# Optimization experiments

Hardware: AMD Instinct MI355X
Metric: run time of the kernel (lower is better)

The kernel has to match this reference:

```python
import jax, jax.numpy as jnp
import numpy as np

B, CIN, F, L = 16, 4, 64, 4096
H = CIN * F   # d_model = 256
N = 32        # SSM state size (S4D)

def setup_inputs() -> dict:
    key = jax.random.key(0)
    ks = jax.random.split(key, 9)
    inp = jax.random.normal(ks[0], (B, CIN, F, L), dtype=jnp.float32)
    # S4D parameterization: dt log-uniform in [1e-3, 1e-1], A = -exp(log_A_real) + i*A_imag (S4D-Lin init)
    log_dt = jnp.log(10.0 ** jax.random.uniform(ks[1], (H,), minval=-3.0, maxval=-1.0)).astype(jnp.float32)
    log_A_real = jnp.log(0.5 * jnp.ones((H, N), dtype=jnp.float32))
    A_imag = jnp.broadcast_to(np.pi * jnp.arange(N, dtype=jnp.float32), (H, N)).copy()
    C_real = jax.random.normal(ks[2], (H, N), dtype=jnp.float32) * (0.5 ** 0.5)
    C_imag = jax.random.normal(ks[3], (H, N), dtype=jnp.float32) * (0.5 ** 0.5)
    D = jax.random.normal(ks[4], (H,), dtype=jnp.float32)
    W_out = jax.random.normal(ks[5], (H, H), dtype=jnp.float32) / jnp.sqrt(H).astype(jnp.float32)
    b_out = jnp.zeros((H,), dtype=jnp.float32)
    return {"inp": inp, "log_dt": log_dt, "log_A_real": log_A_real, "A_imag": A_imag,
            "C_real": C_real, "C_imag": C_imag, "D": D, "W_out": W_out, "b_out": b_out}

def _s4d_kernel(log_dt, log_A_real, A_imag, C_real, C_imag, length):
    dt = jnp.exp(log_dt)                              # (H,)
    A = -jnp.exp(log_A_real) + 1j * A_imag            # (H,N) complex
    dtA = A * dt[:, None]                             # (H,N)
    C = C_real + 1j * C_imag                          # (H,N)
    Ct = C * (jnp.exp(dtA) - 1.0) / A                 # ZOH discretization of B*C
    l = jnp.arange(length, dtype=jnp.float32)
    vand = jnp.exp(dtA[:, :, None] * l)               # (H,N,L) Vandermonde of exp(dt*A)
    return 2.0 * jnp.einsum('hn,hnl->hl', Ct, vand).real  # (H,L) float

def reference(inp, log_dt, log_A_real, A_imag, C_real, C_imag, D, W_out, b_out):
    b, cin, f, l = inp.shape
    # transpose(2,3) then transpose(1,2): (B,C,F,L) -> (B,L,C,F) -> reshape (B,L,H)
    x = jnp.transpose(inp, (0, 3, 1, 2)).reshape(b, l, cin * f)
    u = jnp.transpose(x, (0, 2, 1))                   # (B,H,L)
    K = _s4d_kernel(log_dt, log_A_real, A_imag, C_real, C_imag, l)  # (H,L)
    n = 2 * l
    y = jnp.fft.irfft(jnp.fft.rfft(u, n) * jnp.fft.rfft(K, n), n)[..., :l]  # causal conv
    y = y + D[:, None] * u                            # skip connection
    y = jnp.transpose(y, (0, 2, 1))                   # (B,L,H)
    y = jax.nn.gelu(y)                                # S4Block default activation
    y = y @ W_out.T + b_out                           # output linear, final_act='id'
    # transpose(1,2) then reshape: (B,L,H) -> (B,H,L) -> (B,C,F,L)
    return jnp.transpose(y, (0, 2, 1)).reshape(b, cin, f, l)
```

## Files before the change

### kernel.cpp

```cpp
#include <hip/hip_runtime.h>
#include <hip/hip_bf16.h>
#include <cstdint>

#define S4_H 256
#define S4_N 32
#define S4_L 4096
#define S4_B 16
#define S4_T 64
#define S4_C 64

typedef __attribute__((ext_vector_type(8))) short bf16x8;
typedef __attribute__((ext_vector_type(4))) float f32x4;

__device__ __forceinline__ uint32_t s4_f2bf(float f) {
    uint32_t u = __float_as_uint(f);
    return (u + 0x7fffu + ((u >> 16) & 1u)) >> 16;
}

__device__ __forceinline__ float s4_gelu(float x) {
    float x3 = x * x * x;
    float z = 1.5957691216057308f * fmaf(0.044715f, x3, x);
    float e = __expf(-z);
    return x / (1.0f + e);
}

__device__ __forceinline__ float s4_rowsum32(float v) {
    v += __int_as_float(__builtin_amdgcn_update_dpp(0, __float_as_int(v), 0x111, 0xf, 0xf, false));
    v += __int_as_float(__builtin_amdgcn_update_dpp(0, __float_as_int(v), 0x112, 0xf, 0xf, false));
    v += __int_as_float(__builtin_amdgcn_update_dpp(0, __float_as_int(v), 0x114, 0xf, 0xf, false));
    v += __int_as_float(__builtin_amdgcn_update_dpp(0, __float_as_int(v), 0x118, 0xf, 0xf, false));
    v += __int_as_float(__builtin_amdgcn_update_dpp(0, __float_as_int(v), 0x142, 0xf, 0xf, false));
    return v;
}

__global__ __launch_bounds__(64) void s4_tab_kernel(
        const float* __restrict__ log_dt, const float* __restrict__ log_A_real,
        const float* __restrict__ A_imag, const float* __restrict__ C_real,
        const float* __restrict__ C_imag,
        float* __restrict__ wT, ushort* __restrict__ Ebf,
        ushort* __restrict__ TMbf, ushort* __restrict__ Vbf) {
    const int h = blockIdx.x, tid = threadIdx.x, n = tid & 31;
    __shared__ float Ksh[S4_T];
    const int idx = h * 32 + n;
    float dt = expf(log_dt[h]);
    float Ar = -expf(log_A_real[idx]);
    float Ai = A_imag[idx];
    float er = expf(dt * Ar);
    float wr = er * cosf(dt * Ai);
    float wi = er * sinf(dt * Ai);
    float inv = 1.0f / (Ar * Ar + Ai * Ai);
    float mr = wr - 1.0f, mi = wi;
    float qr = (mr * Ar + mi * Ai) * inv;
    float qi = (mi * Ar - mr * Ai) * inv;
    float Cr = C_real[idx], Ci = C_imag[idx];
    float cr = 2.0f * (Cr * qr - Ci * qi);
    float ci = -2.0f * (Cr * qi + Ci * qr);
    ushort* Eh = Ebf + h * 4096;
    ushort* Vh = Vbf + h * 4096;
    float pr = 1.0f, pi = 0.0f;
    for (int t = 0; t < S4_T; ++t) {
        if (tid < 32) {
            Eh[(2 * n) * 64 + (63 - t)]     = (ushort)s4_f2bf(pr);
            Eh[(2 * n + 1) * 64 + (63 - t)] = (ushort)s4_f2bf(pi);
        }
        float kt = s4_rowsum32(fmaf(cr, pr, ci * pi));
        if (tid == 31) Ksh[t] = kt;
        float Qr = pr * wr - pi * wi;
        float Qi = pr * wi + pi * wr;
        if (tid < 32) {
            Vh[t * 64 + 2 * n]     = (ushort)s4_f2bf(fmaf(cr, Qr, ci * Qi));
            Vh[t * 64 + 2 * n + 1] = (ushort)s4_f2bf(fmaf(ci, Qr, -cr * Qi));
        }
        pr = Qr; pi = Qi;
    }
    if (tid < 32) { wT[idx] = pr; wT[8192 + idx] = pi; }
    __syncthreads();
    ushort* TMh = TMbf + h * 4096;
    for (int e = tid; e < 4096; e += 64) {
        int to = e >> 6, ti = e & 63;
        TMh[e] = (ti <= to) ? (ushort)s4_f2bf(Ksh[to - ti]) : (ushort)0;
    }
}

__global__ __launch_bounds__(256) void s4_wconv(const float* __restrict__ W,
                                               ushort* __restrict__ Wp) {
    const int m = threadIdx.x, ko = blockIdx.x;
    const float* src = W + (size_t)m * S4_H + ko * 8;
    float4 a = *(const float4*)src;
    float4 b = *(const float4*)(src + 4);
    uint4 pk;
    pk.x = s4_f2bf(a.x) | (s4_f2bf(a.y) << 16);
    pk.y = s4_f2bf(a.z) | (s4_f2bf(a.w) << 16);
    pk.z = s4_f2bf(b.x) | (s4_f2bf(b.y) << 16);
    pk.w = s4_f2bf(b.z) | (s4_f2bf(b.w) << 16);
    *(uint4*)(Wp + ((size_t)ko * S4_H + m) * 8) = pk;
}

__global__ __launch_bounds__(256, 6) void s4_scan_fused(
        const float* __restrict__ u, const float* __restrict__ wT,
        const ushort* __restrict__ Ebf, const ushort* __restrict__ TMbf,
        const ushort* __restrict__ Vbf, const float* __restrict__ D,
        uint32_t* __restrict__ g) {
    __shared__ char UXbfB[8192];
    __shared__ float Ssh[64][66];
    const int tid = threadIdx.x;
    const int bh = blockIdx.x;
    const int h = bh & (S4_H - 1);
    const int w = tid >> 6, lane = tid & 63;
    const int l15 = lane & 15, lg = lane >> 4;

    const float* up = u + (size_t)bh * S4_L;
    {
        const float4* uf = (const float4*)up;
        #pragma unroll
        for (int j = 0; j < 4; ++j) {
            int i = j * 256 + tid;
            float4 v = uf[i];
            uint2 pk;
            pk.x = s4_f2bf(v.x) | (s4_f2bf(v.y) << 16);
            pk.y = s4_f2bf(v.z) | (s4_f2bf(v.w) << 16);
            int o = i * 8;
            *(uint2*)(UXbfB + (o ^ (((o >> 7) & 7) << 4))) = pk;
        }
    }
    const int arow = 16 * w + l15;
    const size_t tb = (size_t)h * 4096 + (size_t)arow * 64 + lg * 8;
    bf16x8 eA0 = *(const bf16x8*)(Ebf + tb);
    bf16x8 eA1 = *(const bf16x8*)(Ebf + tb + 32);
    bf16x8 tA0 = *(const bf16x8*)(TMbf + tb);
    bf16x8 tA1 = *(const bf16x8*)(TMbf + tb + 32);
    bf16x8 vA0 = *(const bf16x8*)(Vbf + tb);
    bf16x8 vA1 = *(const bf16x8*)(Vbf + tb + 32);
    __syncthreads();

    bf16x8 ufr[4][2];
    uint2 eu[4];
    const int t0 = 16 * w + lg * 4;
    #pragma unroll
    for (int ct = 0; ct < 4; ++ct) {
        int c = ct * 16 + l15;
        int swz = (c & 7) << 4;
        ufr[ct][0] = *(const bf16x8*)(UXbfB + c * 128 + ((lg * 16) ^ swz));
        ufr[ct][1] = *(const bf16x8*)(UXbfB + c * 128 + ((64 + lg * 16) ^ swz));
        eu[ct] = *(const uint2*)(UXbfB + c * 128 + ((t0 * 2) ^ swz));
        f32x4 acc = {0.f, 0.f, 0.f, 0.f};
        acc = __builtin_amdgcn_mfma_f32_16x16x32_bf16(eA0, ufr[ct][0], acc, 0, 0, 0);
        acc = __builtin_amdgcn_mfma_f32_16x16x32_bf16(eA1, ufr[ct][1], acc, 0, 0, 0);
        *(f32x4*)(&Ssh[c][16 * w + lg * 4]) = acc;
    }
    __syncthreads();

    f32x4 yac[4];
    #pragma unroll
    for (int ct = 0; ct < 4; ++ct) {
        f32x4 y = {0.f, 0.f, 0.f, 0.f};
        y = __builtin_amdgcn_mfma_f32_16x16x32_bf16(tA0, ufr[ct][0], y, 0, 0, 0);
        if (w >= 2)
            y = __builtin_amdgcn_mfma_f32_16x16x32_bf16(tA1, ufr[ct][1], y, 0, 0, 0);
        yac[ct] = y;
    }

    if (tid < 32) {
        float wtr = wT[h * 32 + tid], wti = wT[8192 + h * 32 + tid];
        float xr = 0.f, xi = 0.f;
        #pragma unroll
        for (int c = 0; c < S4_C; ++c) {
            int o = c * 128 + tid * 4;
            *(uint32_t*)(UXbfB + (o ^ (((c & 7) << 4)))) = s4_f2bf(xr) | (s4_f2bf(xi) << 16);
            float2 s2 = *(const float2*)(&Ssh[c][2 * tid]);
            float nr2 = fmaf(wtr, xr, fmaf(-wti, xi, s2.x));
            float ni2 = fmaf(wtr, xi, fmaf(wti, xr, s2.y));
            xr = nr2; xi = ni2;
        }
    }
    __syncthreads();

    const float Dh = D[h];
    uint32_t* gp = g + (size_t)bh * (S4_L / 2);
    #pragma unroll
    for (int ct = 0; ct < 4; ++ct) {
        int c = ct * 16 + l15;
        int swz = (c & 7) << 4;
        bf16x8 xb0 = *(const bf16x8*)(UXbfB + c * 128 + ((lg * 16) ^ swz));
        bf16x8 xb1 = *(const bf16x8*)(UXbfB + c * 128 + ((64 + lg * 16) ^ swz));
        f32x4 y = yac[ct];
        y = __builtin_amdgcn_mfma_f32_16x16x32_bf16(vA0, xb0, y, 0, 0, 0);
        y = __builtin_amdgcn_mfma_f32_16x16x32_bf16(vA1, xb1, y, 0, 0, 0);
        uint2 upk = eu[ct];
        float u0 = __uint_as_float(upk.x << 16);
        float u1 = __uint_as_float(upk.x & 0xffff0000u);
        float u2 = __uint_as_float(upk.y << 16);
        float u3 = __uint_as_float(upk.y & 0xffff0000u);
        float g0 = s4_gelu(fmaf(Dh, u0, y[0]));
        float g1 = s4_gelu(fmaf(Dh, u1, y[1]));
        float g2 = s4_gelu(fmaf(Dh, u2, y[2]));
        float g3 = s4_gelu(fmaf(Dh, u3, y[3]));
        uint2 opk;
        opk.x = s4_f2bf(g0) | (s4_f2bf(g1) << 16);
        opk.y = s4_f2bf(g2) | (s4_f2bf(g3) << 16);
        *(uint2*)(gp + (c * 64 + t0) / 2) = opk;
    }
}

__global__ __launch_bounds__(256) void s4_gemm_mfma(
        const ushort* __restrict__ g,
        const ushort* __restrict__ Wp,
        const float* __restrict__ bias, float* __restrict__ out) {
    __shared__ char GlB[32768];
    const int tid = threadIdx.x;
    const int wv = tid >> 6, lane = tid & 63;
    const int l15 = lane & 15, lg = lane >> 4;
    const int b = blockIdx.y;
    const int l0 = blockIdx.x << 6;

    {
        const int ho = tid >> 3, lp = tid & 7;
        const ushort* gb = g + ((size_t)(b * S4_H) + ho * 8) * S4_L + l0;
        #pragma unroll
        for (int it = 0; it < 4; ++it) {
            const int ll = 2 * (lp + 8 * it);
            uint32_t r[8];
            #pragma unroll
            for (int i = 0; i < 8; ++i)
                r[i] = *(const uint32_t*)(gb + (size_t)i * S4_L + ll);
            uint4 lo, hi;
            lo.x = (r[0] & 0xffffu) | (r[1] << 16);
            lo.y = (r[2] & 0xffffu) | (r[3] << 16);
            lo.z = (r[4] & 0xffffu) | (r[5] << 16);
            lo.w = (r[6] & 0xffffu) | (r[7] << 16);
            hi.x = (r[0] >> 16) | (r[1] & 0xffff0000u);
            hi.y = (r[2] >> 16) | (r[3] & 0xffff0000u);
            hi.z = (r[4] >> 16) | (r[5] & 0xffff0000u);
            hi.w = (r[6] >> 16) | (r[7] & 0xffff0000u);
            *(uint4*)(GlB + ll * 512 + ((ho ^ (ll & 15)) << 4)) = lo;
            *(uint4*)(GlB + (ll + 1) * 512 + ((ho ^ ((ll + 1) & 15)) << 4)) = hi;
        }
    }
    __syncthreads();

    f32x4 acc[4][4] = {};
    const ushort* wpl = Wp + (size_t)(64 * wv + l15) * 8;
    #pragma unroll
    for (int kb = 0; kb < 8; ++kb) {
        const int ko = kb * 4 + lg;
        bf16x8 aF[4], bF[4];
        #pragma unroll
        for (int i = 0; i < 4; ++i)
            aF[i] = *(const bf16x8*)(wpl + ((size_t)ko * S4_H + i * 16) * 8);
        #pragma unroll
        for (int j = 0; j < 4; ++j)
            bF[j] = *(const bf16x8*)(GlB + (j * 16 + l15) * 512 + ((ko ^ l15) << 4));
        #pragma unroll
        for (int i = 0; i < 4; ++i)
            #pragma unroll
            for (int j = 0; j < 4; ++j)
                acc[i][j] = __builtin_amdgcn_mfma_f32_16x16x32_bf16(aF[i], bF[j], acc[i][j], 0, 0, 0);
    }

    float* ob = out + ((size_t)(b * S4_H) + 64 * wv) * S4_L + l0;
    #pragma unroll
    for (int i = 0; i < 4; ++i) {
        #pragma unroll
        for (int jj = 0; jj < 4; ++jj) {
            const int mrow = i * 16 + lg * 4 + jj;
            const float bv = bias[64 * wv + mrow];
            float* orow = ob + (size_t)mrow * S4_L + l15;
            #pragma unroll
            for (int j = 0; j < 4; ++j)
                orow[j * 16] = acc[i][j][jj] + bv;
        }
    }
}

extern "C" void kernel_launch(void* const* d_in, const int* in_sizes, int n_in,
                              void* d_out, int out_size, void* d_ws, size_t ws_size,
                              hipStream_t stream) {
    const float* inp        = (const float*)d_in[0];
    const float* log_dt     = (const float*)d_in[1];
    const float* log_A_real = (const float*)d_in[2];
    const float* A_imag     = (const float*)d_in[3];
    const float* C_real     = (const float*)d_in[4];
    const float* C_imag     = (const float*)d_in[5];
    const float* D          = (const float*)d_in[6];
    const float* W_out      = (const float*)d_in[7];
    const float* b_out      = (const float*)d_in[8];
    float* out = (float*)d_out;

    char* wsc = (char*)d_ws;
    size_t off = 0;
    float* wT     = (float*)(wsc + off);  off += (64 << 10);
    ushort* Ebf   = (ushort*)(wsc + off); off += (2 << 20);
    ushort* TMbf  = (ushort*)(wsc + off); off += (2 << 20);
    ushort* Vbf   = (ushort*)(wsc + off); off += (2 << 20);
    ushort* Wp    = (ushort*)(wsc + off); off += (128 << 10);
    uint32_t* g   = (uint32_t*)(wsc + off);

    hipLaunchKernelGGL(s4_tab_kernel, dim3(S4_H), dim3(64), 0, stream,
                       log_dt, log_A_real, A_imag, C_real, C_imag, wT, Ebf, TMbf, Vbf);
    hipLaunchKernelGGL(s4_wconv, dim3(32), dim3(256), 0, stream, W_out, Wp);
    hipLaunchKernelGGL(s4_scan_fused, dim3(S4_B * S4_H), dim3(256), 0, stream,
                       inp, wT, Ebf, TMbf, Vbf, D, g);
    hipLaunchKernelGGL(s4_gemm_mfma, dim3(S4_L / 64, S4_B), dim3(256), 0, stream,
                       (const ushort*)g, Wp, b_out, out);
}
```

Measured before the change: 75.54 us.

## Assign one (batch,channel) row per wavefront in chunked scan kernel

```diff
diff --git a/kernel.cpp b/kernel.cpp
--- a/kernel.cpp
+++ b/kernel.cpp
@@ -96,109 +96,113 @@
     *(uint4*)(Wp + ((size_t)ko * S4_H + m) * 8) = pk;
 }
 
-__global__ __launch_bounds__(256, 6) void s4_scan_fused(
+__global__ __launch_bounds__(256, 3) void s4_scan_fused(
         const float* __restrict__ u, const float* __restrict__ wT,
         const ushort* __restrict__ Ebf, const ushort* __restrict__ TMbf,
         const ushort* __restrict__ Vbf, const float* __restrict__ D,
         uint32_t* __restrict__ g) {
-    __shared__ char UXbfB[8192];
-    __shared__ float Ssh[64][66];
+    __shared__ char Ssh[4][8192];
     const int tid = threadIdx.x;
-    const int bh = blockIdx.x;
+    const int wv = tid >> 6, lane = tid & 63;
+    const int l15 = lane & 15, lg = lane >> 4;
+    const int bh = blockIdx.x * 4 + wv;
     const int h = bh & (S4_H - 1);
-    const int w = tid >> 6, lane = tid & 63;
-    const int l15 = lane & 15, lg = lane >> 4;
-
+    char* sbase = Ssh[wv];
     const float* up = u + (size_t)bh * S4_L;
-    {
-        const float4* uf = (const float4*)up;
-        #pragma unroll
-        for (int j = 0; j < 4; ++j) {
-            int i = j * 256 + tid;
-            float4 v = uf[i];
+
+    bf16x8 ufr[4][2];
+    #pragma unroll
+    for (int ct = 0; ct < 4; ++ct) {
+        #pragma unroll
+        for (int q = 0; q < 2; ++q) {
+            const float* p = up + (ct * 16 + l15) * 64 + q * 32 + lg * 8;
+            float4 v0 = *(const float4*)p;
+            float4 v1 = *(const float4*)(p + 4);
+            union { uint32_t w[4]; bf16x8 v; } pk;
+            pk.w[0] = s4_f2bf(v0.x) | (s4_f2bf(v0.y) << 16);
+            pk.w[1] = s4_f2bf(v0.z) | (s4_f2bf(v0.w) << 16);
+            pk.w[2] = s4_f2bf(v1.x) | (s4_f2bf(v1.y) << 16);
+            pk.w[3] = s4_f2bf(v1.z) | (s4_f2bf(v1.w) << 16);
+            ufr[ct][q] = pk.v;
+        }
+    }
+
+    const size_t trow = (size_t)h * 4096 + (size_t)l15 * 64 + lg * 8;
+    f32x4 sac[4][4] = {};
+    #pragma unroll
+    for (int q = 0; q < 2; ++q)
+        #pragma unroll
+        for (int mt = 0; mt < 4; ++mt) {
+            bf16x8 eA = *(const bf16x8*)(Ebf + trow + mt * 1024 + q * 32);
+            #pragma unroll
+            for (int nt = 0; nt < 4; ++nt)
+                sac[mt][nt] = __builtin_amdgcn_mfma_f32_16x16x32_bf16(eA, ufr[nt][q], sac[mt][nt], 0, 0, 0);
+        }
+    #pragma unroll
+    for (int mt = 0; mt < 4; ++mt)
+        #pragma unroll
+        for (int nt = 0; nt < 4; ++nt) {
+            int c = nt * 16 + l15;
+            int byt = (c * 128 + mt * 32 + lg * 8) ^ ((c & 7) << 4);
             uint2 pk;
-            pk.x = s4_f2bf(v.x) | (s4_f2bf(v.y) << 16);
-            pk.y = s4_f2bf(v.z) | (s4_f2bf(v.w) << 16);
-            int o = i * 8;
-            *(uint2*)(UXbfB + (o ^ (((o >> 7) & 7) << 4))) = pk;
-        }
-    }
-    const int arow = 16 * w + l15;
-    const size_t tb = (size_t)h * 4096 + (size_t)arow * 64 + lg * 8;
-    bf16x8 eA0 = *(const bf16x8*)(Ebf + tb);
-    bf16x8 eA1 = *(const bf16x8*)(Ebf + tb + 32);
-    bf16x8 tA0 = *(const bf16x8*)(TMbf + tb);
-    bf16x8 tA1 = *(const bf16x8*)(TMbf + tb + 32);
-    bf16x8 vA0 = *(const bf16x8*)(Vbf + tb);
-    bf16x8 vA1 = *(const bf16x8*)(Vbf + tb + 32);
-    __syncthreads();
-
-    bf16x8 ufr[4][2];
-    uint2 eu[4];
-    const int t0 = 16 * w + lg * 4;
+            pk.x = s4_f2bf(sac[mt][nt][0]) | (s4_f2bf(sac[mt][nt][1]) << 16);
+            pk.y = s4_f2bf(sac[mt][nt][2]) | (s4_f2bf(sac[mt][nt][3]) << 16);
+            *(uint2*)(sbase + byt) = pk;
+        }
+
+    if (lane < 32) {
+        float wtr = wT[h * 32 + lane], wti = wT[8192 + h * 32 + lane];
+        float xr = 0.f, xi = 0.f;
+        #pragma unroll 16
+        for (int c = 0; c < S4_C; ++c) {
+            int off = (c * 128 + lane * 4) ^ ((c & 7) << 4);
+            uint32_t sp = *(uint32_t*)(sbase + off);
+            *(uint32_t*)(sbase + off) = s4_f2bf(xr) | (s4_f2bf(xi) << 16);
+            float sr = __uint_as_float(sp << 16);
+            float si = __uint_as_float(sp & 0xffff0000u);
+            float nr = fmaf(wtr, xr, fmaf(-wti, xi, sr));
+            float ni = fmaf(wtr, xi, fmaf(wti, xr, si));
+            xr = nr; xi = ni;
+        }
+    }
+
+    bf16x8 xb[4][2];
     #pragma unroll
     for (int ct = 0; ct < 4; ++ct) {
         int c = ct * 16 + l15;
-        int swz = (c & 7) << 4;
-        ufr[ct][0] = *(const bf16x8*)(UXbfB + c * 128 + ((lg * 16) ^ swz));
-        ufr[ct][1] = *(const bf16x8*)(UXbfB + c * 128 + ((64 + lg * 16) ^ swz));
-        eu[ct] = *(const uint2*)(UXbfB + c * 128 + ((t0 * 2) ^ swz));
-        f32x4 acc = {0.f, 0.f, 0.f, 0.f};
-        acc = __builtin_amdgcn_mfma_f32_16x16x32_bf16(eA0, ufr[ct][0], acc, 0, 0, 0);
-        acc = __builtin_amdgcn_mfma_f32_16x16x32_bf16(eA1, ufr[ct][1], acc, 0, 0, 0);
-        *(f32x4*)(&Ssh[c][16 * w + lg * 4]) = acc;
-    }
-    __syncthreads();
-
-    f32x4 yac[4];
-    #pragma unroll
-    for (int ct = 0; ct < 4; ++ct) {
-        f32x4 y = {0.f, 0.f, 0.f, 0.f};
-        y = __builtin_amdgcn_mfma_f32_16x16x32_bf16(tA0, ufr[ct][0], y, 0, 0, 0);
-        if (w >= 2)
-            y = __builtin_amdgcn_mfma_f32_16x16x32_bf16(tA1, ufr[ct][1], y, 0, 0, 0);
-        yac[ct] = y;
-    }
-
-    if (tid < 32) {
-        float wtr = wT[h * 32 + tid], wti = wT[8192 + h * 32 + tid];
-        float xr = 0.f, xi = 0.f;
-        #pragma unroll
-        for (int c = 0; c < S4_C; ++c) {
-            int o = c * 128 + tid * 4;
-            *(uint32_t*)(UXbfB + (o ^ (((c & 7) << 4)))) = s4_f2bf(xr) | (s4_f2bf(xi) << 16);
-            float2 s2 = *(const float2*)(&Ssh[c][2 * tid]);
-            float nr2 = fmaf(wtr, xr, fmaf(-wti, xi, s2.x));
-            float ni2 = fmaf(wtr, xi, fmaf(wti, xr, s2.y));
-            xr = nr2; xi = ni2;
-        }
-    }
-    __syncthreads();
+        #pragma unroll
+        for (int q = 0; q < 2; ++q)
+            xb[ct][q] = *(const bf16x8*)(sbase + ((c * 128 + q * 64 + lg * 16) ^ ((c & 7) << 4)));
+    }
 
     const float Dh = D[h];
     uint32_t* gp = g + (size_t)bh * (S4_L / 2);
     #pragma unroll
-    for (int ct = 0; ct < 4; ++ct) {
-        int c = ct * 16 + l15;
-        int swz = (c & 7) << 4;
-        bf16x8 xb0 = *(const bf16x8*)(UXbfB + c * 128 + ((lg * 16) ^ swz));
-        bf16x8 xb1 = *(const bf16x8*)(UXbfB + c * 128 + ((64 + lg * 16) ^ swz));
-        f32x4 y = yac[ct];
-        y = __builtin_amdgcn_mfma_f32_16x16x32_bf16(vA0, xb0, y, 0, 0, 0);
-        y = __builtin_amdgcn_mfma_f32_16x16x32_bf16(vA1, xb1, y, 0, 0, 0);
-        uint2 upk = eu[ct];
-        float u0 = __uint_as_float(upk.x << 16);
-        float u1 = __uint_as_float(upk.x & 0xffff0000u);
-        float u2 = __uint_as_float(upk.y << 16);
-        float u3 = __uint_as_float(upk.y & 0xffff0000u);
-        float g0 = s4_gelu(fmaf(Dh, u0, y[0]));
-        float g1 = s4_gelu(fmaf(Dh, u1, y[1]));
-        float g2 = s4_gelu(fmaf(Dh, u2, y[2]));
-        float g3 = s4_gelu(fmaf(Dh, u3, y[3]));
-        uint2 opk;
-        opk.x = s4_f2bf(g0) | (s4_f2bf(g1) << 16);
-        opk.y = s4_f2bf(g2) | (s4_f2bf(g3) << 16);
-        *(uint2*)(gp + (c * 64 + t0) / 2) = opk;
+    for (int mt = 0; mt < 4; ++mt) {
+        bf16x8 t0f = *(const bf16x8*)(TMbf + trow + mt * 1024);
+        bf16x8 t1f = {};
+        if (mt >= 2) t1f = *(const bf16x8*)(TMbf + trow + mt * 1024 + 32);
+        bf16x8 v0f = *(const bf16x8*)(Vbf + trow + mt * 1024);
+        bf16x8 v1f = *(const bf16x8*)(Vbf + trow + mt * 1024 + 32);
+        #pragma unroll
+        for (int ct = 0; ct < 4; ++ct) {
+            f32x4 y = {0.f, 0.f, 0.f, 0.f};
+            y = __builtin_amdgcn_mfma_f32_16x16x32_bf16(t0f, ufr[ct][0], y, 0, 0, 0);
+            if (mt >= 2)
+                y = __builtin_amdgcn_mfma_f32_16x16x32_bf16(t1f, ufr[ct][1], y, 0, 0, 0);
+            y = __builtin_amdgcn_mfma_f32_16x16x32_bf16(v0f, xb[ct][0], y, 0, 0, 0);
+            y = __builtin_amdgcn_mfma_f32_16x16x32_bf16(v1f, xb[ct][1], y, 0, 0, 0);
+            int c = ct * 16 + l15;
+            float4 uv = *(const float4*)(up + c * 64 + mt * 16 + lg * 4);
+            float g0 = s4_gelu(fmaf(Dh, uv.x, y[0]));
+            float g1 = s4_gelu(fmaf(Dh, uv.y, y[1]));
+            float g2 = s4_gelu(fmaf(Dh, uv.z, y[2]));
+            float g3 = s4_gelu(fmaf(Dh, uv.w, y[3]));
+            uint2 opk;
+            opk.x = s4_f2bf(g0) | (s4_f2bf(g1) << 16);
+            opk.y = s4_f2bf(g2) | (s4_f2bf(g3) << 16);
+            *(uint2*)(gp + c * 32 + mt * 8 + lg * 2) = opk;
+        }
     }
 }
 
@@ -298,7 +302,7 @@
     hipLaunchKernelGGL(s4_tab_kernel, dim3(S4_H), dim3(64), 0, stream,
                        log_dt, log_A_real, A_imag, C_real, C_imag, wT, Ebf, TMbf, Vbf);
     hipLaunchKernelGGL(s4_wconv, dim3(32), dim3(256), 0, stream, W_out, Wp);
-    hipLaunchKernelGGL(s4_scan_fused, dim3(S4_B * S4_H), dim3(256), 0, stream,
+    hipLaunchKernelGGL(s4_scan_fused, dim3(S4_B * S4_H / 4), dim3(256), 0, stream,
                        inp, wT, Ebf, TMbf, Vbf, D, g);
     hipLaunchKernelGGL(s4_gemm_mfma, dim3(S4_L / 64, S4_B), dim3(256), 0, stream,
                        (const ushort*)g, Wp, b_out, out);
```

Result: slower. 86.56 us (+14.6%).
